# Performance work log

Hardware: AMD Instinct MI355X
Metric: run time of the kernel (lower is better)

## Reference

```python
import jax, jax.numpy as jnp
import numpy as np

B, N, IN_F = 4, 2048, 256
H, HEAD_DIM = 8, 32  # out_features=256, concat=True -> head_dim=32
ALPHA = 0.2
MASK_VAL = -9e15


def setup_inputs() -> dict:
    key = jax.random.key(0)
    k1, k2, k3, k4 = jax.random.split(key, 4)
    x = jax.random.normal(k1, (B, N, IN_F), dtype=jnp.float32)
    adj = jax.random.randint(k2, (B, N, N), 0, 2, dtype=jnp.int32)
    # xavier_uniform for W [H, in, head_dim]: gain=1, fan_in=in, fan_out=head_dim
    limW = float(np.sqrt(6.0 / (IN_F + HEAD_DIM)))
    W = jax.random.uniform(k3, (H, IN_F, HEAD_DIM), dtype=jnp.float32, minval=-limW, maxval=limW)
    # xavier_uniform for a [H, 2*head_dim]: fan_in=2*head_dim, fan_out=H (2D tensor)
    lima = float(np.sqrt(6.0 / (H + 2 * HEAD_DIM)))
    a = jax.random.uniform(k4, (H, 2 * HEAD_DIM), dtype=jnp.float32, minval=-lima, maxval=lima)
    return {"x": x, "adj": adj, "W": W, "a": a}


def reference(x, adj, W, a):
    # x: [B, N, F], adj: [B, N, N], W: [H, F, D], a: [H, 2D]
    D = W.shape[-1]
    Wh = jnp.einsum('bnf,hfd->bhnd', x, W)                     # [B,H,N,D]
    a_src, a_dst = a[:, :D], a[:, D:]
    # additive score e_ij = a_src . Wh_i + a_dst . Wh_j (equivalent to concat+matmul)
    e_i = jnp.einsum('bhnd,hd->bhn', Wh, a_src)                # [B,H,N]
    e_j = jnp.einsum('bhnd,hd->bhn', Wh, a_dst)                # [B,H,N]
    scores = e_i[:, :, :, None] + e_j[:, :, None, :]           # [B,H,N,N]
    scores = jnp.where(scores > 0, scores, ALPHA * scores)     # LeakyReLU
    scores = jnp.where(adj[:, None, :, :] == 0, MASK_VAL, scores)
    probs = jax.nn.softmax(scores, axis=-1)                    # [B,H,N,N]
    h = jnp.einsum('bhij,bhjd->bhid', probs, Wh)               # [B,H,N,D]
    b, n = x.shape[0], x.shape[1]
    return h.transpose(0, 2, 1, 3).reshape(b, n, h.shape[1] * D)  # concat heads
```

## Files before the change

### kernel.cpp

```cpp
#include <hip/hip_runtime.h>

#define BB 4
#define NN 2048
#define INF 256
#define HH 8
#define DD 32
#define LOG2E 1.4426950408889634f

typedef __attribute__((ext_vector_type(8))) short short8;
typedef __attribute__((ext_vector_type(4))) float f32x4;

__device__ __forceinline__ unsigned short bf16_rne(float v) {
    unsigned b = __float_as_uint(v);
    return (unsigned short)((b + 0x7fffu + ((b >> 16) & 1u)) >> 16);
}
__device__ __forceinline__ unsigned short bf16_rhu(float v) {
    return (unsigned short)((__float_as_uint(v) + 0x8000u) >> 16);
}

__global__ __launch_bounds__(256) void wprep_kernel(
    const float* __restrict__ W, const float* __restrict__ a,
    float* __restrict__ we_g, unsigned short* __restrict__ wT)
{
    const int bb = blockIdx.x, t = threadIdx.x;
    if (bb < 16) {
        const int h = bb & 7, sel = bb >> 3;
        const float* wr = W + ((size_t)(h * INF + t)) * DD;
        const float* av = a + h * 2 * DD + sel * DD;
        float acc = 0.f;
        #pragma unroll
        for (int d = 0; d < DD; ++d) acc += wr[d] * av[d];
        we_g[bb * INF + t] = acc * LOG2E;
    }
    #pragma unroll
    for (int r2 = 0; r2 < 8; ++r2) {
        int row = bb * 8 + r2;
        int h = row >> 5, d = row & 31;
        wT[row * INF + t] = bf16_rhu(W[((size_t)(h * INF + t)) * DD + d]);
    }
}

__global__ __launch_bounds__(256) void ek_kernel(
    const float* __restrict__ x, const float* __restrict__ we_g,
    float* __restrict__ esrc, unsigned* __restrict__ ejP)
{
    __shared__ __align__(16) float xs[16 * 260];
    __shared__ __align__(16) float weld2[16 * 260];
    const int t = threadIdx.x;
    const int tile = blockIdx.x & 127, b = blockIdx.x >> 7;
    const int n0 = tile * 16;

    #pragma unroll
    for (int p = 0; p < 4; ++p) {
        int flat = p * 1024 + t * 4;
        int row = flat >> 8, col = flat & 255;
        f32x4 g = *(const f32x4*)&x[((size_t)(b * NN + n0 + row)) * INF + col];
        *(f32x4*)&xs[row * 260 + col] = g;
    }
    #pragma unroll
    for (int p = 0; p < 4; ++p) {
        int flat = p * 1024 + t * 4;
        int k = flat >> 8, f = flat & 255;
        f32x4 g = *(const f32x4*)&we_g[flat];
        *(f32x4*)&weld2[(f >> 4) * 260 + k * 16 + (f & 15)] = g;
    }
    __syncthreads();

    const int row = t >> 4, c = t & 15;
    f32x4 xv[4];
    #pragma unroll
    for (int i = 0; i < 4; ++i)
        xv[i] = *(const f32x4*)&xs[row * 260 + c * 16 + i * 4];

    float keep = 0.f;
    #pragma unroll
    for (int k = 0; k < 16; ++k) {
        float s = 0.f;
        #pragma unroll
        for (int i = 0; i < 4; ++i) {
            f32x4 w4 = *(const f32x4*)&weld2[c * 260 + k * 16 + i * 4];
            s += xv[i][0]*w4[0] + xv[i][1]*w4[1] + xv[i][2]*w4[2] + xv[i][3]*w4[3];
        }
        s += __shfl_xor(s, 1, 64);
        s += __shfl_xor(s, 2, 64);
        s += __shfl_xor(s, 4, 64);
        s += __shfl_xor(s, 8, 64);
        keep = (c == k) ? s : keep;
    }
    const int n = n0 + row;
    if (c < 8) {
        esrc[(b * 8 + c) * NN + n] = keep;
    } else {
        float Ej  = __builtin_amdgcn_exp2f(keep);
        float Ej5 = __builtin_amdgcn_exp2f(0.2f * keep);
        ejP[(b * 8 + (c - 8)) * NN + n] =
            ((unsigned)bf16_rne(Ej) << 16) | (unsigned)bf16_rne(Ej5);
    }
}

__global__ __launch_bounds__(256) void whk_kernel(
    const float* __restrict__ x, const unsigned short* __restrict__ wT,
    unsigned short* __restrict__ whT2)
{
    __shared__ __align__(16) unsigned short xb[64 * 264];
    __shared__ __align__(16) unsigned short wb[64 * 264];
    const int t = threadIdx.x;
    const int hp = blockIdx.x & 3, tl = (blockIdx.x >> 2) & 31, b = blockIdx.x >> 7;
    const int n0 = tl * 64;

    #pragma unroll
    for (int p = 0; p < 16; ++p) {
        int flat = p * 1024 + t * 4;
        int row = flat >> 8, col = flat & 255;
        f32x4 g = *(const f32x4*)&x[((size_t)(b * NN + n0 + row)) * INF + col];
        unsigned a0 = __float_as_uint(g[0]) + 0x8000u;
        unsigned a1 = __float_as_uint(g[1]) + 0x8000u;
        unsigned a2 = __float_as_uint(g[2]) + 0x8000u;
        unsigned a3 = __float_as_uint(g[3]) + 0x8000u;
        uint2 pk;
        pk.x = __builtin_amdgcn_perm(a1, a0, 0x07060302u);
        pk.y = __builtin_amdgcn_perm(a3, a2, 0x07060302u);
        *(uint2*)&xb[row * 264 + col] = pk;
    }
    #pragma unroll
    for (int p = 0; p < 8; ++p) {
        int flat = p * 2048 + t * 8;
        int cc = flat >> 8, f = flat & 255;
        *(short8*)&wb[cc * 264 + f] = *(const short8*)&wT[(hp * 64 + cc) * INF + f];
    }
    __syncthreads();

    const int w = t >> 6, l = t & 63;
    const int ml = l & 15, q = l >> 4;
    f32x4 acc[4] = {};
    const unsigned short* ap = &xb[(w * 16 + ml) * 264 + q * 8];
    #pragma unroll
    for (int k0 = 0; k0 < INF; k0 += 32) {
        short8 A = *(const short8*)&ap[k0];
        #pragma unroll
        for (int c16 = 0; c16 < 4; ++c16) {
            short8 Bf = *(const short8*)&wb[(c16 * 16 + ml) * 264 + q * 8 + k0];
            acc[c16] = __builtin_amdgcn_mfma_f32_16x16x32_bf16(A, Bf, acc[c16], 0, 0, 0);
        }
    }
    __syncthreads();

    unsigned short* ldsC = xb;
    #pragma unroll
    for (int c16 = 0; c16 < 4; ++c16)
        #pragma unroll
        for (int r = 0; r < 4; ++r) {
            int col = c16 * 16 + ml;
            int rt  = w * 16 + q * 4 + r;
            ldsC[col * 72 + rt] = bf16_rhu(acc[c16][r]);
        }
    __syncthreads();

    #pragma unroll
    for (int p = 0; p < 2; ++p) {
        int g = p * 256 + t;
        int d = g & 31, jo = (g >> 5) & 7, h2 = g >> 8;
        short8 vv = *(const short8*)&ldsC[(h2 * 32 + d) * 72 + jo * 8];
        int bh = b * 8 + hp * 2 + h2;
        *(short8*)&whT2[(((size_t)bh * 256 + tl * 8 + jo) * 32 + d) * 8] = vv;
    }
}

__global__ __launch_bounds__(1024, 4) void attn_kernel(
    const int* __restrict__ adj, const unsigned short* __restrict__ whT2,
    const float* __restrict__ esrc, const unsigned* __restrict__ ejP,
    float* __restrict__ out)
{
    __shared__ __align__(16) unsigned bits[2][2][32][4];
    __shared__ __align__(16) float cmb[8][64][24];
    const int t = threadIdx.x, v = t >> 6, l = t & 63;
    const int h = v & 7, js = v >> 3;
    const int ml = l & 15, q = l >> 4;
    const int it = blockIdx.x & 63, b = blockIdx.x >> 6;
    const int i0 = it * 32;
    const int bh = b * HH + h;

    const float ei0 = esrc[bh * NN + i0 + ml];
    const float ei1 = esrc[bh * NN + i0 + 16 + ml];
    const float Ei0  = __builtin_amdgcn_exp2f(ei0);
    const float Ei05 = __builtin_amdgcn_exp2f(0.2f * ei0);
    const float Ei1  = __builtin_amdgcn_exp2f(ei1);
    const float Ei15 = __builtin_amdgcn_exp2f(0.2f * ei1);

    const unsigned* epP = ejP + bh * NN + js * 1024;
    const unsigned short* whb = whT2 + ((size_t)bh * 256 + js * 128) * 256;

    auto stage = [&](int c2, int buf) {
        #pragma unroll
        for (int u = 0; u < 4; ++u) {
            int uid = v * 4 + u;
            int row = uid & 31, half = uid >> 5;
            const int* g = adj + ((size_t)(b * NN + i0 + row)) * NN
                               + half * 1024 + c2 * 128 + l;
            int a0 = g[0], a1 = g[64];
            unsigned long long m0 = __ballot(a0 != 0);
            unsigned long long m1 = __ballot(a1 != 0);
            if (l == 0) {
                uint4 pv = make_uint4((unsigned)m0, (unsigned)(m0 >> 32),
                                      (unsigned)m1, (unsigned)(m1 >> 32));
                *(uint4*)&bits[buf][half][row][0] = pv;
            }
        }
    };

    const short8 ones = {0x3F80, 0x3F80, 0x3F80, 0x3F80, 0x3F80, 0x3F80, 0x3F80, 0x3F80};
    f32x4 acc00 = {}, acc01 = {}, acc10 = {}, acc11 = {}, accD0 = {}, accD1 = {};

    stage(0, 0);
    for (int c = 0; c < 8; ++c) {
        __syncthreads();
        if (c < 7) stage(c + 1, (c + 1) & 1);
        const int buf = c & 1;
        unsigned w0a[4], w1a[4];
        *(uint4*)w0a = *(const uint4*)&bits[buf][js][ml][0];
        *(uint4*)w1a = *(const uint4*)&bits[buf][js][16 + ml][0];
        const unsigned* epc = epP + c * 128;
        #pragma unroll
        for (int k = 0; k < 4; ++k) {
            const int jb = k * 32 + q * 8;
            uint4 epA = *(const uint4*)&epc[jb];
            uint4 epB = *(const uint4*)&epc[jb + 4];
            const unsigned short* wp = whb + (size_t)(c * 16 + k * 4 + q) * 256;
            short8 B0 = *(const short8*)&wp[ml * 8];
            short8 B1 = *(const short8*)&wp[(16 + ml) * 8];
            unsigned st0 = w0a[k] >> (q * 8);
            unsigned st1 = w1a[k] >> (q * 8);
            union { unsigned u[4]; short8 s; } f0, f1;
            const unsigned* ea = &epA.x;
            const unsigned* eb = &epB.x;
            #pragma unroll
            for (int pp = 0; pp < 4; ++pp) {
                unsigned pkA = (pp < 2) ? ea[2 * pp]     : eb[2 * pp - 4];
                unsigned pkB = (pp < 2) ? ea[2 * pp + 1] : eb[2 * pp - 3];
                float EjA = __uint_as_float(pkA & 0xffff0000u);
                float FjA = __uint_as_float(pkA << 16);
                float EjB = __uint_as_float(pkB & 0xffff0000u);
                float FjB = __uint_as_float(pkB << 16);
                unsigned mA0 = (unsigned)__builtin_amdgcn_sbfe(st0, 2 * pp, 1);
                unsigned mB0 = (unsigned)__builtin_amdgcn_sbfe(st0, 2 * pp + 1, 1);
                unsigned mA1 = (unsigned)__builtin_amdgcn_sbfe(st1, 2 * pp, 1);
                unsigned mB1 = (unsigned)__builtin_amdgcn_sbfe(st1, 2 * pp + 1, 1);
                float pA0 = fmaxf(EjA * Ei0, FjA * Ei05);
                float pB0 = fmaxf(EjB * Ei0, FjB * Ei05);
                float pA1 = fmaxf(EjA * Ei1, FjA * Ei15);
                float pB1 = fmaxf(EjB * Ei1, FjB * Ei15);
                f0.u[pp] = __builtin_amdgcn_perm(__float_as_uint(pB0) & mB0,
                                                 __float_as_uint(pA0) & mA0,
                                                 0x07060302u);
                f1.u[pp] = __builtin_amdgcn_perm(__float_as_uint(pB1) & mB1,
                                                 __float_as_uint(pA1) & mA1,
                                                 0x07060302u);
            }
            acc00 = __builtin_amdgcn_mfma_f32_16x16x32_bf16(f0.s, B0, acc00, 0, 0, 0);
            acc01 = __builtin_amdgcn_mfma_f32_16x16x32_bf16(f0.s, B1, acc01, 0, 0, 0);
            accD0 = __builtin_amdgcn_mfma_f32_16x16x32_bf16(f0.s, ones, accD0, 0, 0, 0);
            acc10 = __builtin_amdgcn_mfma_f32_16x16x32_bf16(f1.s, B0, acc10, 0, 0, 0);
            acc11 = __builtin_amdgcn_mfma_f32_16x16x32_bf16(f1.s, B1, acc11, 0, 0, 0);
            accD1 = __builtin_amdgcn_mfma_f32_16x16x32_bf16(f1.s, ones, accD1, 0, 0, 0);
        }
    }

    float* myc = &cmb[h][l][0];
    if (js == 1) {
        *(f32x4*)&myc[0]  = acc00; *(f32x4*)&myc[4]  = acc01;
        *(f32x4*)&myc[8]  = acc10; *(f32x4*)&myc[12] = acc11;
        *(f32x4*)&myc[16] = accD0; *(f32x4*)&myc[20] = accD1;
    }
    __syncthreads();
    if (js == 0) {
        f32x4 o00 = *(const f32x4*)&myc[0],  o01 = *(const f32x4*)&myc[4];
        f32x4 o10 = *(const f32x4*)&myc[8],  o11 = *(const f32x4*)&myc[12];
        f32x4 oD0 = *(const f32x4*)&myc[16], oD1 = *(const f32x4*)&myc[20];
        #pragma unroll
        for (int r = 0; r < 4; ++r) {
            int ir0 = i0 + q * 4 + r;
            int ir1 = i0 + 16 + q * 4 + r;
            float inv0 = 1.0f / (accD0[r] + oD0[r]);
            float inv1 = 1.0f / (accD1[r] + oD1[r]);
            size_t ba0 = ((size_t)(b * NN + ir0)) * (HH * DD) + h * DD;
            size_t ba1 = ((size_t)(b * NN + ir1)) * (HH * DD) + h * DD;
            out[ba0 + ml]      = (acc00[r] + o00[r]) * inv0;
            out[ba0 + 16 + ml] = (acc01[r] + o01[r]) * inv0;
            out[ba1 + ml]      = (acc10[r] + o10[r]) * inv1;
            out[ba1 + 16 + ml] = (acc11[r] + o11[r]) * inv1;
        }
    }
}

extern "C" void kernel_launch(void* const* d_in, const int* in_sizes, int n_in,
                              void* d_out, int out_size, void* d_ws, size_t ws_size,
                              hipStream_t stream) {
    (void)in_sizes; (void)n_in; (void)out_size; (void)ws_size;
    const float* x   = (const float*)d_in[0];
    const int*   adj = (const int*)d_in[1];
    const float* W   = (const float*)d_in[2];
    const float* a   = (const float*)d_in[3];
    float* out = (float*)d_out;

    char* ws = (char*)d_ws;
    unsigned short* whT2 = (unsigned short*)ws;
    unsigned short* wT   = (unsigned short*)(ws + (4u << 20));
    float*    esrc = (float*)(ws + (4u << 20) + (128u << 10));
    unsigned* ejP  = (unsigned*)(esrc + BB * HH * NN);
    float*    we_g = (float*)(ejP + BB * HH * NN);

    wprep_kernel<<<dim3(32),  dim3(256), 0, stream>>>(W, a, we_g, wT);
    ek_kernel  <<<dim3(512),  dim3(256), 0, stream>>>(x, we_g, esrc, ejP);
    whk_kernel <<<dim3(512),  dim3(256), 0, stream>>>(x, wT, whT2);
    attn_kernel<<<dim3(256),  dim3(1024), 0, stream>>>(adj, whT2, esrc, ejP, out);
}
```

Baseline: 152.8 us.

## Prefetch adjacency tiles two chunks ahead in registers and pad combine LDS buffer

Splits adjacency staging into a global-load phase into registers and a ballot/commit phase into LDS. Loads are issued two chunks ahead, so global memory latency overlaps with a full chunk of MFMA work instead of stalling right after the barrier. It also pads the cmb shared array row stride from 24 to 25 floats to reduce LDS bank conflicts. The cost is extra registers for the prefetched values, which matters under launch bounds of 1024 threads with 4 blocks.

```diff
diff --git a/kernel.cpp b/kernel.cpp
--- a/kernel.cpp
+++ b/kernel.cpp
@@ -172,7 +172,7 @@
     float* __restrict__ out)
 {
     __shared__ __align__(16) unsigned bits[2][2][32][4];
-    __shared__ __align__(16) float cmb[8][64][24];
+    __shared__ __align__(16) float cmb[8][64][25];
     const int t = threadIdx.x, v = t >> 6, l = t & 63;
     const int h = v & 7, js = v >> 3;
     const int ml = l & 15, q = l >> 4;
@@ -190,16 +190,29 @@
     const unsigned* epP = ejP + bh * NN + js * 1024;
     const unsigned short* whb = whT2 + ((size_t)bh * 256 + js * 128) * 256;
 
-    auto stage = [&](int c2, int buf) {
+    const int* gbase[4];
+    #pragma unroll
+    for (int u = 0; u < 4; ++u) {
+        int uid = v * 4 + u;
+        int row = uid & 31, half = uid >> 5;
+        gbase[u] = adj + ((size_t)(b * NN + i0 + row)) * NN + half * 1024 + l;
+    }
+
+    auto stage_load = [&](int c2, int* ra, int* rb) {
+        #pragma unroll
+        for (int u = 0; u < 4; ++u) {
+            const int* g = gbase[u] + c2 * 128;
+            ra[u] = g[0];
+            rb[u] = g[64];
+        }
+    };
+    auto stage_commit = [&](const int* ra, const int* rb, int buf) {
         #pragma unroll
         for (int u = 0; u < 4; ++u) {
             int uid = v * 4 + u;
             int row = uid & 31, half = uid >> 5;
-            const int* g = adj + ((size_t)(b * NN + i0 + row)) * NN
-                               + half * 1024 + c2 * 128 + l;
-            int a0 = g[0], a1 = g[64];
-            unsigned long long m0 = __ballot(a0 != 0);
-            unsigned long long m1 = __ballot(a1 != 0);
+            unsigned long long m0 = __ballot(ra[u] != 0);
+            unsigned long long m1 = __ballot(rb[u] != 0);
             if (l == 0) {
                 uint4 pv = make_uint4((unsigned)m0, (unsigned)(m0 >> 32),
                                       (unsigned)m1, (unsigned)(m1 >> 32));
@@ -211,10 +224,21 @@
     const short8 ones = {0x3F80, 0x3F80, 0x3F80, 0x3F80, 0x3F80, 0x3F80, 0x3F80, 0x3F80};
     f32x4 acc00 = {}, acc01 = {}, acc10 = {}, acc11 = {}, accD0 = {}, accD1 = {};
 
-    stage(0, 0);
+    int rA0[4], rA1[4], rB0[4], rB1[4];
+    stage_load(0, rA0, rA1);
+    stage_load(1, rB0, rB1);
+    stage_commit(rA0, rA1, 0);
+
     for (int c = 0; c < 8; ++c) {
         __syncthreads();
-        if (c < 7) stage(c + 1, (c + 1) & 1);
+        if (c < 7) {
+            if (c & 1) stage_commit(rA0, rA1, (c + 1) & 1);
+            else       stage_commit(rB0, rB1, (c + 1) & 1);
+        }
+        if (c < 6) {
+            if (c & 1) stage_load(c + 2, rB0, rB1);
+            else       stage_load(c + 2, rA0, rA1);
+        }
         const int buf = c & 1;
         unsigned w0a[4], w1a[4];
         *(uint4*)w0a = *(const uint4*)&bits[buf][js][ml][0];
```

After: 148.2 us. -3.0%, faster.

## Precompute adjacency bitmask in a separate kernel and read it directly in attention

Applied to the files above, without the earlier changes.

Adds a prebit kernel that packs the int32 adjacency matrix into a global bitmask with wave ballots. The attention kernel then loads its mask words straight from global memory, so the in-loop adj staging, the shared bits buffer and the per-chunk __syncthreads are gone. The cmb shared array is padded to 25 floats to avoid bank conflicts. This costs an extra kernel launch and a separate full pass over adj, but the bitmask is 32x smaller and the attention loop no longer needs block-level sync.

```diff
diff --git a/kernel.cpp b/kernel.cpp
--- a/kernel.cpp
+++ b/kernel.cpp
@@ -40,6 +40,31 @@
     }
 }
 
+__global__ __launch_bounds__(256) void prebit_kernel(
+    const int* __restrict__ adj, unsigned* __restrict__ bitsG)
+{
+    const int t = threadIdx.x, w = t >> 6, l = t & 63;
+    const int sb = blockIdx.x * 256 + w * 64;
+    #pragma unroll 1
+    for (int i = 0; i < 16; ++i) {
+        int s0 = sb + i * 4;
+        int a0[4];
+        #pragma unroll
+        for (int u = 0; u < 4; ++u) {
+            int s = s0 + u;
+            a0[u] = adj[((size_t)(s >> 5)) * 2048 + (s & 31) * 64 + l];
+        }
+        #pragma unroll
+        for (int u = 0; u < 4; ++u) {
+            int s = s0 + u;
+            unsigned long long m = __ballot(a0[u] != 0);
+            if (l == 0)
+                *(uint2*)&bitsG[((size_t)(s >> 5)) * 64 + (s & 31) * 2] =
+                    make_uint2((unsigned)m, (unsigned)(m >> 32));
+        }
+    }
+}
+
 __global__ __launch_bounds__(256) void ek_kernel(
     const float* __restrict__ x, const float* __restrict__ we_g,
     float* __restrict__ esrc, unsigned* __restrict__ ejP)
@@ -60,9 +85,9 @@
     #pragma unroll
     for (int p = 0; p < 4; ++p) {
         int flat = p * 1024 + t * 4;
-        int k = flat >> 8, f = flat & 255;
         f32x4 g = *(const f32x4*)&we_g[flat];
-        *(f32x4*)&weld2[(f >> 4) * 260 + k * 16 + (f & 15)] = g;
+        int f = flat & 255;
+        *(f32x4*)&weld2[(f >> 4) * 260 + (flat >> 8) * 16 + (f & 15)] = g;
     }
     __syncthreads();
 
@@ -167,12 +192,11 @@
 }
 
 __global__ __launch_bounds__(1024, 4) void attn_kernel(
-    const int* __restrict__ adj, const unsigned short* __restrict__ whT2,
+    const unsigned* __restrict__ bitsG, const unsigned short* __restrict__ whT2,
     const float* __restrict__ esrc, const unsigned* __restrict__ ejP,
     float* __restrict__ out)
 {
-    __shared__ __align__(16) unsigned bits[2][2][32][4];
-    __shared__ __align__(16) float cmb[8][64][24];
+    __shared__ __align__(16) float cmb[8][64][25];
     const int t = threadIdx.x, v = t >> 6, l = t & 63;
     const int h = v & 7, js = v >> 3;
     const int ml = l & 15, q = l >> 4;
@@ -189,36 +213,17 @@
 
     const unsigned* epP = ejP + bh * NN + js * 1024;
     const unsigned short* whb = whT2 + ((size_t)bh * 256 + js * 128) * 256;
-
-    auto stage = [&](int c2, int buf) {
-        #pragma unroll
-        for (int u = 0; u < 4; ++u) {
-            int uid = v * 4 + u;
-            int row = uid & 31, half = uid >> 5;
-            const int* g = adj + ((size_t)(b * NN + i0 + row)) * NN
-                               + half * 1024 + c2 * 128 + l;
-            int a0 = g[0], a1 = g[64];
-            unsigned long long m0 = __ballot(a0 != 0);
-            unsigned long long m1 = __ballot(a1 != 0);
-            if (l == 0) {
-                uint4 pv = make_uint4((unsigned)m0, (unsigned)(m0 >> 32),
-                                      (unsigned)m1, (unsigned)(m1 >> 32));
-                *(uint4*)&bits[buf][half][row][0] = pv;
-            }
-        }
-    };
+    const unsigned* bg0 = bitsG + ((size_t)(b * NN + i0 + ml)) * 64 + js * 32;
+    const unsigned* bg1 = bitsG + ((size_t)(b * NN + i0 + 16 + ml)) * 64 + js * 32;
 
     const short8 ones = {0x3F80, 0x3F80, 0x3F80, 0x3F80, 0x3F80, 0x3F80, 0x3F80, 0x3F80};
     f32x4 acc00 = {}, acc01 = {}, acc10 = {}, acc11 = {}, accD0 = {}, accD1 = {};
 
-    stage(0, 0);
+    #pragma unroll 2
     for (int c = 0; c < 8; ++c) {
-        __syncthreads();
-        if (c < 7) stage(c + 1, (c + 1) & 1);
-        const int buf = c & 1;
         unsigned w0a[4], w1a[4];
-        *(uint4*)w0a = *(const uint4*)&bits[buf][js][ml][0];
-        *(uint4*)w1a = *(const uint4*)&bits[buf][js][16 + ml][0];
+        *(uint4*)w0a = *(const uint4*)&bg0[c * 4];
+        *(uint4*)w1a = *(const uint4*)&bg1[c * 4];
         const unsigned* epc = epP + c * 128;
         #pragma unroll
         for (int k = 0; k < 4; ++k) {
@@ -308,9 +313,11 @@
     float*    esrc = (float*)(ws + (4u << 20) + (128u << 10));
     unsigned* ejP  = (unsigned*)(esrc + BB * HH * NN);
     float*    we_g = (float*)(ejP + BB * HH * NN);
-
-    wprep_kernel<<<dim3(32),  dim3(256), 0, stream>>>(W, a, we_g, wT);
-    ek_kernel  <<<dim3(512),  dim3(256), 0, stream>>>(x, we_g, esrc, ejP);
-    whk_kernel <<<dim3(512),  dim3(256), 0, stream>>>(x, wT, whT2);
-    attn_kernel<<<dim3(256),  dim3(1024), 0, stream>>>(adj, whT2, esrc, ejP, out);
-}
+    unsigned* bitsG = (unsigned*)(we_g + 16 * INF);
+
+    wprep_kernel <<<dim3(32),   dim3(256),  0, stream>>>(W, a, we_g, wT);
+    prebit_kernel<<<dim3(1024), dim3(256),  0, stream>>>(adj, bitsG);
+    ek_kernel    <<<dim3(512),  dim3(256),  0, stream>>>(x, we_g, esrc, ejP);
+    whk_kernel   <<<dim3(512),  dim3(256),  0, stream>>>(x, wT, whT2);
+    attn_kernel  <<<dim3(256),  dim3(1024), 0, stream>>>(bitsG, whT2, esrc, ejP, out);
+}
```

Measured after the change: 166.4 us. 8.9% more time.
